# Kernel tuning notes

Hardware: AMD Instinct MI355X
Metric: run time of the kernel (lower is better)

The kernel has to match this reference:

```python
import jax, jax.numpy as jnp
import numpy as np

POS_THR = 0.5      # ROI_POSITIVE_THR
NEG_THR = 0.1      # ROI_NEGATIVE_THR
N_SAMPLES = 256    # ROI_SAMPLES
FG_RATIO = 0.25    # ROI_SAMPLE_RATIO
L1W = 1.0          # RPN.L1WEIGHT_INTERSECTION
NUM_FG = int(N_SAMPLES * FG_RATIO)


def _make_boxes(kxy, kwh, shape):
    # valid [x1,y1,x2,y2] boxes in an ~800px image
    xy = jax.random.uniform(kxy, shape[:-1] + (2,)) * 800.0
    wh = jax.random.uniform(kwh, shape[:-1] + (2,)) * 200.0 + 1.0
    return jnp.concatenate([xy, xy + wh], axis=-1)


def setup_inputs() -> dict:
    key = jax.random.key(0)
    k1, k2, k3, k4 = jax.random.split(key, 4)
    proposals = _make_boxes(k1, k2, (16, 16384, 4))  # [B, N, 4]
    gt_boxes = _make_boxes(k3, k4, (16, 128, 4))     # [B, G, 4]
    return {"proposals": proposals, "gt_boxes": gt_boxes}


def _centrehw(b):
    # [x1,y1,x2,y2] -> [cx,cy,w,h]
    x1, y1, x2, y2 = b[..., 0], b[..., 1], b[..., 2], b[..., 3]
    return jnp.stack([(x1 + x2) * 0.5, (y1 + y2) * 0.5, x2 - x1, y2 - y1], axis=-1)


def _targets(gt_c, roi_c):
    dx = (gt_c[..., 0] - roi_c[..., 0]) / roi_c[..., 2]
    dy = (gt_c[..., 1] - roi_c[..., 1]) / roi_c[..., 3]
    dw = jnp.log(gt_c[..., 2] / roi_c[..., 2])
    dh = jnp.log(gt_c[..., 3] / roi_c[..., 3])
    return jnp.stack([dx, dy, dw, dh], axis=-1)


def _iou(prop, gt):
    # prop [B,N,4], gt [B,G,4] -> IoU [B,N,G]
    p = prop[:, :, None, :]
    g = gt[:, None, :, :]
    ix1 = jnp.maximum(p[..., 0], g[..., 0])
    iy1 = jnp.maximum(p[..., 1], g[..., 1])
    ix2 = jnp.minimum(p[..., 2], g[..., 2])
    iy2 = jnp.minimum(p[..., 3], g[..., 3])
    inter = jnp.clip(ix2 - ix1, 0.0) * jnp.clip(iy2 - iy1, 0.0)
    ap = (p[..., 2] - p[..., 0]) * (p[..., 3] - p[..., 1])
    ag = (g[..., 2] - g[..., 0]) * (g[..., 3] - g[..., 1])
    return inter / jnp.maximum(ap + ag - inter, 1e-8)


def _forward(proposals, gt_boxes):
    B, N, _ = proposals.shape
    iou = _iou(proposals, gt_boxes)                       # [B,N,G]
    max_iou = iou.max(axis=-1)                            # [B,N]
    argmax_gt = iou.argmax(axis=-1).astype(jnp.int32)     # [B,N]
    # classify: 1=fg, 0=bg, -1=ignore
    labels = jnp.where(max_iou >= POS_THR, 1,
                       jnp.where(max_iou < NEG_THR, 0, -1)).astype(jnp.int32)
    # randsample: keep <= NUM_FG positives (random), fill rest with negatives.
    r = jax.random.uniform(jax.random.key(1), (B, N))
    pos = labels == 1
    r_pos = jnp.where(pos, r, -1.0)
    order = jnp.argsort(-r_pos, axis=1)
    ranks = jnp.argsort(order, axis=1)                    # rank among positives by r
    pos_sel = pos & (ranks < NUM_FG)
    prio = jnp.where(pos_sel, 3.0 + r,
                     jnp.where(labels == 0, 2.0 + r,
                               jnp.where(pos, 1.0 + r, r)))
    _, idx = jax.lax.top_k(prio, N_SAMPLES)               # [B,S] sampled proposal ids
    batch_labels = jnp.maximum(jnp.take_along_axis(labels, idx, axis=1), 0)  # [B,S]
    roi_batch = jnp.take_along_axis(proposals, idx[..., None], axis=1)       # [B,S,4]
    sel_gt = jnp.take_along_axis(argmax_gt, idx, axis=1)                     # [B,S]
    gt_batch = jnp.take_along_axis(gt_boxes, sel_gt[..., None], axis=1)      # [B,S,4]
    bbox_targets = _targets(_centrehw(gt_batch), _centrehw(roi_batch))       # [B,S,4]
    in_w = jnp.where((batch_labels == 1)[..., None], L1W, 0.0)
    in_w = jnp.broadcast_to(in_w, bbox_targets.shape)
    out_w = (in_w > 0).astype(jnp.float32)
    return roi_batch, batch_labels, bbox_targets, in_w, out_w


def reference(proposals, gt_boxes):
    return _forward(proposals, gt_boxes)
```

## Files before the change

kernel.cpp:

```cpp
#include <hip/hip_runtime.h>
#include <stdint.h>

#define BATCH 16
#define NPROP 16384
#define NGT   128
#define NSAMP 256
#define NFG   64
#define GCAP  512
#define PCAP  8192
#define HCAP  4096
#define NBLK  64
#define BPB   256
#define LOGB  8

typedef unsigned long long ull;

__device__ __forceinline__ void thr_block(uint32_t c0, uint32_t c1,
                                          uint32_t* o0, uint32_t* o1) {
    const uint32_t k0 = 0u, k1 = 1u, ks2 = 0x1BD11BDBu;
    uint32_t x0 = c0 + k0, x1 = c1 + k1;
#define RND(d) { x0 += x1; x1 = (x1 << d) | (x1 >> (32 - d)); x1 ^= x0; }
    RND(13) RND(15) RND(26) RND(6)   x0 += k1;  x1 += ks2 + 1u;
    RND(17) RND(29) RND(16) RND(24)  x0 += ks2; x1 += k0 + 2u;
    RND(13) RND(15) RND(26) RND(6)   x0 += k0;  x1 += k1 + 3u;
    RND(17) RND(29) RND(16) RND(24)  x0 += k1;  x1 += ks2 + 4u;
    RND(13) RND(15) RND(26) RND(6)   x0 += ks2; x1 += k0 + 5u;
#undef RND
    *o0 = x0; *o1 = x1;
}

__device__ __forceinline__ uint32_t thr_part_xor(uint32_t f) {
    uint32_t a, b; thr_block(0u, f, &a, &b);
    return a ^ b;
}

__global__ void __launch_bounds__(256) k_compute(
    const float* __restrict__ props, const float* __restrict__ gts,
    ull* __restrict__ lists, uint32_t* __restrict__ cntblk)
{
#pragma clang fp contract(off)
    const int b = blockIdx.y;
    const int blk = blockIdx.x;
    const int tid = threadIdx.x;
    const int n = blk * BPB + tid;
    __shared__ float4 g4[NGT];
    __shared__ uint32_t wc[3][4], we_s[3][4];
    if (tid < NGT)
        g4[tid] = ((const float4*)gts)[(size_t)b * NGT + tid];
    __syncthreads();
    const float4 pb = ((const float4*)props)[(size_t)b * NPROP + n];
    const float ap = (pb.z - pb.x) * (pb.w - pb.y);
    float best = -1.0f; int bg = 0;
    #pragma unroll 4
    for (int i = 0; i < NGT; ++i) {
        const float4 gb = g4[i];
        float ag = (gb.z - gb.x) * (gb.w - gb.y);
        float w  = fmaxf(fminf(pb.z, gb.z) - fmaxf(pb.x, gb.x), 0.0f);
        float hh = fmaxf(fminf(pb.w, gb.w) - fmaxf(pb.y, gb.y), 0.0f);
        float inter = w * hh;
        float un = fmaxf(ap + ag - inter, 1e-8f);
        float iou = inter / un;
        if (iou > best) { best = iou; bg = i; }
    }
    uint32_t lab = (best >= 0.5f) ? 2u : ((best < 0.1f) ? 1u : 0u);
    const uint32_t f = (uint32_t)b * NPROP + (uint32_t)n;
    uint32_t mant = thr_part_xor(f) >> 9;
    ull entry = ((ull)(lab == 2u) << 44) | ((ull)mant << 21)
              | ((ull)(16383u - (uint32_t)n) << 7) | (ull)(uint32_t)bg;

    bool cP = (lab == 2u);
    bool cN = (lab == 1u);
    bool cI = (lab == 0u);
    ull mP = __ballot(cP), mN = __ballot(cN), mI = __ballot(cI);
    const int w = tid >> 6;
    const uint32_t lane = (uint32_t)tid & 63u;
    if (lane == 0) {
        wc[0][w] = (uint32_t)__popcll(mP);
        wc[1][w] = (uint32_t)__popcll(mN);
        wc[2][w] = (uint32_t)__popcll(mI);
    }
    __syncthreads();
    if (tid < 3) {
        uint32_t e = 0;
        #pragma unroll
        for (int i = 0; i < 4; i++) { we_s[tid][i] = e; e += wc[tid][i]; }
        cntblk[((size_t)b * NBLK + blk) * 4 + tid] = e;
    }
    __syncthreads();
    ull lt = lane ? (~0ull >> (64u - lane)) : 0ull;
    ull* slab = lists + (size_t)b * 4 * NPROP;
    const uint32_t segB = (uint32_t)blk * BPB;
    if (cP) slab[0 * NPROP + segB + we_s[0][w] + (uint32_t)__popcll(mP & lt)] = entry;
    if (cN) slab[1 * NPROP + segB + we_s[1][w] + (uint32_t)__popcll(mN & lt)] = entry;
    if (cI) slab[2 * NPROP + segB + we_s[2][w] + (uint32_t)__popcll(mI & lt)] = entry;
}

__global__ void __launch_bounds__(1024) k_select(
    const float* __restrict__ props, const float* __restrict__ gts,
    const ull* __restrict__ lists, const uint32_t* __restrict__ cntblk,
    float* __restrict__ out)
{
#pragma clang fp contract(off)
    const int b = blockIdx.x;
    const int tid = threadIdx.x;
    const int wid = tid >> 6;
    const uint32_t lane = (uint32_t)tid & 63u;
    __shared__ ull      dpos[PCAP];
    __shared__ ull      dneg[HCAP];
    __shared__ uint32_t histA[2048];
    __shared__ uint32_t histB[2048];
    __shared__ ull      gatA[GCAP];
    __shared__ ull      gatB[GCAP];
    __shared__ ull      selk[NSAMP];
    __shared__ uint32_t sela[NSAMP];
    __shared__ uint32_t bc[NBLK * 4];
    __shared__ uint32_t preP[NBLK], preN[NBLK], tot[3];
    __shared__ uint32_t shA[3], shB[3], shS[3];
    __shared__ uint32_t gcA, gcB, gcnt, selc;
    __shared__ ull sh_thrA, sh_thrB, sh_thr;

    const ull* Spos = lists + ((size_t)b * 4 + 0) * NPROP;
    const ull* Sneg = lists + ((size_t)b * 4 + 1) * NPROP;
    const ull* Sign = lists + ((size_t)b * 4 + 2) * NPROP;

    if (tid < NBLK * 4) bc[tid] = cntblk[(size_t)b * NBLK * 4 + tid];
    histA[tid] = 0; histA[tid + 1024] = 0;
    histB[tid] = 0; histB[tid + 1024] = 0;
    if (tid == 0) { gcA = 0; gcB = 0; gcnt = 0; selc = 0; }
    __syncthreads();
    if (wid < 3) {
        uint32_t own = bc[lane * 4 + (uint32_t)wid];
        uint32_t v = own;
        #pragma unroll
        for (int off = 1; off < 64; off <<= 1) {
            uint32_t t = (uint32_t)__shfl_up((int)v, off);
            if (lane >= (uint32_t)off) v += t;
        }
        if (wid == 0) preP[lane] = v - own;
        else if (wid == 1) preN[lane] = v - own;
        if (lane == 63) tot[wid] = v;
    }
    __syncthreads();
    const uint32_t npos = tot[0], nneg = tot[1], nig = tot[2];
    const uint32_t npn  = npos + nneg;
    const uint32_t c3   = (npos < NFG) ? npos : NFG;
    const uint32_t k2   = NSAMP - c3;
    const bool dP = (npos <= PCAP), dH = (nneg <= HCAP);
    const bool fast0 = (npn >= NSAMP) && (c3 + nneg >= NSAMP) && dP && dH;

    auto keyA_of = [](ull e) -> ull {
        return (((e >> 21) & 0x7FFFFFull) << 14) | ((e >> 7) & 0x3FFFull);
    };
    auto keyB_neg = [](ull ent) -> ull {
        uint32_t mant = (uint32_t)((ent >> 21) & 0x7FFFFFull);
        uint32_t invn = (uint32_t)((ent >> 7) & 0x3FFFull);
        float r = __uint_as_float(0x3F800000u | mant) - 1.0f;
        float prio = 2.0f + r;
        return (((ull)__float_as_uint(prio)) << 14) | (ull)invn;
    };
    auto keyB_ign = [](ull ent) -> ull {
        uint32_t mant = (uint32_t)((ent >> 21) & 0x7FFFFFull);
        uint32_t invn = (uint32_t)((ent >> 7) & 0x3FFFull);
        float r = __uint_as_float(0x3F800000u | mant) - 1.0f;
        float prio = 0.0f + r;
        return (((ull)__float_as_uint(prio)) << 14) | (ull)invn;
    };
    ull thrA = 0;
    auto keyB_pos = [&](ull ent) -> ull {
        uint32_t mant = (uint32_t)((ent >> 21) & 0x7FFFFFull);
        uint32_t invn = (uint32_t)((ent >> 7) & 0x3FFFull);
        float r = __uint_as_float(0x3F800000u | mant) - 1.0f;
        uint32_t cls = (keyA_of(ent) >= thrA) ? 3u : 1u;
        float prio = (float)cls + r;
        return (((ull)__float_as_uint(prio)) << 14) | (ull)invn;
    };
    auto push = [&](ull key, ull ent, uint32_t fg) {
        uint32_t s = atomicAdd(&selc, 1u);
        if (s < NSAMP) { selk[s] = key; sela[s] = (fg << 7) | (uint32_t)(ent & 0x7Full); }
    };

    for (int s4 = 0; s4 < 4; ++s4) {
        uint32_t seg = (uint32_t)(wid * 4 + s4);
        if (dP) {
            uint32_t c = bc[seg * 4 + 0], bb = preP[seg];
            for (uint32_t i = lane; i < c; i += 64) {
                ull ent = Spos[seg * BPB + i];
                dpos[bb + i] = ent;
                if (fast0 && npos > NFG)
                    atomicAdd(&histA[(uint32_t)(keyA_of(ent) >> 26) & 2047u], 1u);
            }
        }
        if (dH) {
            uint32_t c = bc[seg * 4 + 1], bb = preN[seg];
            for (uint32_t i = lane; i < c; i += 64) {
                ull ent = Sneg[seg * BPB + i];
                dneg[bb + i] = ent;
                if (fast0)
                    atomicAdd(&histB[(uint32_t)(keyB_neg(ent) >> 26) & 2047u], 1u);
            }
        }
    }
    __syncthreads();

    auto locW = [&](const uint32_t* h, uint32_t k, uint32_t* o3) {
        uint32_t cs = 0;
        if (lane < 32) {
            const uint32_t base = lane * 64u;
            #pragma unroll 8
            for (uint32_t i = 0; i < 64; i++) cs += h[base + ((i + lane) & 63u)];
        }
        uint32_t s = cs;
        #pragma unroll
        for (int off = 1; off < 32; off <<= 1) {
            uint32_t t = __shfl_down(s, off);
            if (lane + off < 32) s += t;
        }
        uint32_t sExcl = s - cs;
        bool cond = (lane < 32) && (sExcl < k) && (k <= s);
        ull ball = __ballot(cond);
        uint32_t cstar = (uint32_t)(__ffsll((unsigned long long)ball) - 1);
        uint32_t kc_ = (uint32_t)__shfl((int)(k - sExcl), (int)cstar);
        uint32_t val = h[cstar * 64u + lane];
        uint32_t fi = val;
        #pragma unroll
        for (int off = 1; off < 64; off <<= 1) {
            uint32_t t = __shfl_down(fi, off);
            if (lane + off < 64) fi += t;
        }
        uint32_t fExcl = fi - val;
        bool cond2 = (fExcl < kc_) && (kc_ <= fi);
        ull ball2 = __ballot(cond2);
        uint32_t bstar = (uint32_t)(__ffsll((unsigned long long)ball2) - 1);
        if (lane == bstar) { o3[0] = cstar * 64u + lane; o3[1] = kc_ - fExcl; o3[2] = val; }
    };

    bool fast = fast0;
    if (fast) {
        if (wid == 0 && npos > NFG) locW(histA, NFG, shA);
        if (wid == 1)               locW(histB, k2,  shB);
        __syncthreads();
        if ((npos > NFG && shA[2] > GCAP) || (shB[2] > GCAP)) fast = false;
    }
    if (fast) {
        if (npos > NFG) {
            uint32_t digA = shA[0];
            for (uint32_t j = tid; j < npos; j += 1024) {
                ull k = keyA_of(dpos[j]);
                if (((uint32_t)(k >> 26) & 2047u) == digA) gatA[atomicAdd(&gcA, 1u)] = k;
            }
        }
        {
            uint32_t digB = shB[0];
            for (uint32_t j = tid; j < nneg; j += 1024) {
                ull k = keyB_neg(dneg[j]);
                if (((uint32_t)(k >> 26) & 2047u) == digB) gatB[atomicAdd(&gcB, 1u)] = k;
            }
        }
        __syncthreads();
        if (npos > NFG) {
            if ((uint32_t)tid < gcA) {
                ull x = gatA[tid]; uint32_t r = 0;
                for (uint32_t j = 0; j < gcA; j++) r += (gatA[j] > x);
                if (r == shA[1] - 1) sh_thrA = x;
            }
        } else if (tid == 0) sh_thrA = 0;
        if (tid >= 512 && (uint32_t)(tid - 512) < gcB) {
            ull x = gatB[tid - 512]; uint32_t r = 0;
            for (uint32_t j = 0; j < gcB; j++) r += (gatB[j] > x);
            if (r == shB[1] - 1) sh_thrB = x;
        }
        __syncthreads();
        thrA = sh_thrA;
        const ull thrB = sh_thrB;
        for (uint32_t j = tid; j < npos; j += 1024) {
            ull ent = dpos[j];
            if (keyA_of(ent) >= thrA) push(keyB_pos(ent), ent, 1u);
        }
        for (uint32_t j = tid; j < nneg; j += 1024) {
            ull ent = dneg[j];
            ull k = keyB_neg(ent);
            if (k >= thrB) push(k, ent, 0u);
        }
        __syncthreads();
    }
    if (!fast) {
        const uint32_t MSEG = NBLK * BPB;
        const uint32_t mPos = dP ? npos : MSEG;
        const uint32_t mNeg = dH ? nneg : MSEG;
        auto posEnt = [&](uint32_t j, bool& e) -> ull {
            if (dP) { e = true; return dpos[j]; }
            e = (j & (BPB - 1u)) < bc[(j >> LOGB) * 4 + 0];
            return e ? Spos[j] : 0ull;
        };
        auto negEnt = [&](uint32_t j, bool& e) -> ull {
            if (dH) { e = true; return dneg[j]; }
            e = (j & (BPB - 1u)) < bc[(j >> LOGB) * 4 + 1];
            return e ? Sneg[j] : 0ull;
        };
        auto igEnt = [&](uint32_t j, bool& e) -> ull {
            e = (j & (BPB - 1u)) < bc[(j >> LOGB) * 4 + 2];
            return e ? Sign[j] : 0ull;
        };
        auto radix = [&](auto&& kf, uint32_t m, uint32_t k, int shift) -> ull {
            if (m <= GCAP) {
                if (tid == 0) gcnt = 0;
                __syncthreads();
                for (uint32_t j = tid; j < m; j += 1024) {
                    bool e; ull key = kf(j, e);
                    if (e) { uint32_t s = atomicAdd(&gcnt, 1u); gatA[s] = key; }
                }
                __syncthreads();
                uint32_t gc = gcnt;
                if ((uint32_t)tid < gc) {
                    ull x = gatA[tid]; uint32_t r = 0;
                    for (uint32_t j = 0; j < gc; j++) r += (gatA[j] > x);
                    if (r == k - 1) sh_thr = x;
                }
                __syncthreads();
                return sh_thr;
            }
            ull prefix = 0, mask = 0;
            for (;;) {
                histA[tid] = 0; histA[tid + 1024] = 0;
                __syncthreads();
                for (uint32_t j = tid; j < m; j += 1024) {
                    bool e; ull key = kf(j, e);
                    if (e && ((key ^ prefix) & mask) == 0)
                        atomicAdd(&histA[(uint32_t)(key >> shift) & 2047u], 1u);
                }
                __syncthreads();
                if (tid < 64) locW(histA, k, shS);
                __syncthreads();
                uint32_t dig = shS[0], kk = shS[1], cnt = shS[2];
                prefix |= ((ull)dig) << shift;
                mask   |= 2047ull << shift;
                if (cnt <= GCAP || shift == 0) {
                    if (tid == 0) gcnt = 0;
                    __syncthreads();
                    for (uint32_t j = tid; j < m; j += 1024) {
                        bool e; ull key = kf(j, e);
                        if (e && ((key ^ prefix) & mask) == 0) {
                            uint32_t s = atomicAdd(&gcnt, 1u);
                            if (s < GCAP) gatA[s] = key;
                        }
                    }
                    __syncthreads();
                    uint32_t gc = (gcnt < GCAP) ? gcnt : GCAP;
                    if ((uint32_t)tid < gc) {
                        ull x = gatA[tid]; uint32_t r = 0;
                        for (uint32_t j = 0; j < gc; j++) r += (gatA[j] > x);
                        if (r == kk - 1) sh_thr = x;
                    }
                    __syncthreads();
                    return sh_thr;
                } else {
                    k = kk;
                    shift = (shift >= 11) ? shift - 11 : 0;
                    __syncthreads();
                }
            }
        };

        if (npos > NFG) {
            thrA = radix([&](uint32_t j, bool& e) -> ull {
                ull ent = posEnt(j, e); return keyA_of(ent); }, mPos, NFG, 26);
        }
        uint32_t clsStar = (npn >= NSAMP) ? ((NSAMP <= c3 + nneg) ? 2u : 1u) : 0u;
        ull thrB = 0;
        if (clsStar == 2u) {
            thrB = radix([&](uint32_t j, bool& e) -> ull {
                ull ent = negEnt(j, e); return keyB_neg(ent); }, mNeg, k2, 26);
        } else if (clsStar == 1u) {
            thrB = radix([&](uint32_t j, bool& e) -> ull {
                ull ent = posEnt(j, e);
                ull kb = keyB_pos(ent);
                e = e && ((kb >> 14) < 0x40000000ull);
                return kb; }, mPos, NSAMP - c3 - nneg, 26);
        } else {
            thrB = radix([&](uint32_t j, bool& e) -> ull {
                ull ent = igEnt(j, e); return keyB_ign(ent); }, MSEG, NSAMP - npn, 34);
        }
        __syncthreads();
        for (uint32_t j = tid; j < mPos; j += 1024) {
            bool e; ull ent = posEnt(j, e);
            if (!e) continue;
            ull key = keyB_pos(ent);
            if (clsStar == 0u || key >= thrB) push(key, ent, 1u);
        }
        for (uint32_t j = tid; j < mNeg; j += 1024) {
            bool e; ull ent = negEnt(j, e);
            if (!e) continue;
            ull key = keyB_neg(ent);
            if (clsStar == 0u || key >= thrB) push(key, ent, 0u);
        }
        if (clsStar == 0u) {
            for (uint32_t j = tid; j < MSEG; j += 1024) {
                bool e; ull ent = igEnt(j, e);
                if (!e) continue;
                ull key = keyB_ign(ent);
                if (key >= thrB) push(key, ent, 0u);
            }
        }
        __syncthreads();
    }

    if (tid < NSAMP) {
        ull x = selk[tid];
        uint32_t r = 0;
        for (int j = 0; j < NSAMP; j++) r += (selk[j] > x);
        uint32_t n = 16383u - (uint32_t)(x & 0x3FFFull);
        uint32_t aux = sela[tid];
        uint32_t bg = aux & 0x7Fu;
        const int isfg = (int)((aux >> 7) & 1u);
        const float4 pb = ((const float4*)props)[(size_t)b * NPROP + n];
        const float4 gb = ((const float4*)gts)[(size_t)b * NGT + bg];
        const size_t O_ROI = 0;
        const size_t O_LBL = (size_t)BATCH * NSAMP * 4;
        const size_t O_TGT = O_LBL + (size_t)BATCH * NSAMP;
        const size_t O_INW = O_TGT + (size_t)BATCH * NSAMP * 4;
        const size_t O_OUW = O_INW + (size_t)BATCH * NSAMP * 4;
        const size_t row = (size_t)b * NSAMP + r;
        out[O_ROI + row * 4 + 0] = pb.x;
        out[O_ROI + row * 4 + 1] = pb.y;
        out[O_ROI + row * 4 + 2] = pb.z;
        out[O_ROI + row * 4 + 3] = pb.w;
        out[O_LBL + row] = isfg ? 1.0f : 0.0f;
        float rw  = pb.z - pb.x, rh = pb.w - pb.y;
        float gw  = gb.z - gb.x, gh = gb.w - gb.y;
        out[O_TGT + row * 4 + 0] = ((gb.x + gb.z) * 0.5f - (pb.x + pb.z) * 0.5f) / rw;
        out[O_TGT + row * 4 + 1] = ((gb.y + gb.w) * 0.5f - (pb.y + pb.w) * 0.5f) / rh;
        out[O_TGT + row * 4 + 2] = logf(gw / rw);
        out[O_TGT + row * 4 + 3] = logf(gh / rh);
        float wv = isfg ? 1.0f : 0.0f;
        for (int c = 0; c < 4; c++) {
            out[O_INW + row * 4 + c] = wv;
            out[O_OUW + row * 4 + c] = wv;
        }
    }
}

extern "C" void kernel_launch(void* const* d_in, const int* in_sizes, int n_in,
                              void* d_out, int out_size, void* d_ws, size_t ws_size,
                              hipStream_t stream) {
    (void)in_sizes; (void)n_in; (void)out_size; (void)ws_size;
    const float* props = (const float*)d_in[0];
    const float* gts   = (const float*)d_in[1];
    ull* lists = (ull*)d_ws;
    uint32_t* cntblk = (uint32_t*)((char*)d_ws + (size_t)BATCH * 4 * NPROP * 8);
    float* out = (float*)d_out;

    dim3 gridA(NBLK, BATCH);
    k_compute<<<gridA, 256, 0, stream>>>(props, gts, lists, cntblk);
    k_select<<<BATCH, 1024, 0, stream>>>(props, gts, lists, cntblk, out);
}
```

Measured before the change: 99.08 us.

## Split negatives into high/low random-key buckets to shrink select staging

The compute kernel now partitions negative proposals by their random mantissa into a high bucket (mant >= threshold) and a low bucket, writing four lists instead of three. The select kernel stages only the high-key negatives in shared memory, with the staging buffer halved, and runs its histogram radix select over that smaller set when it holds enough candidates. The low bucket is read only in the fallback path. This is meant to cut global reads, atomics and LDS traffic in the select stage, at the cost of an extra ballot and output list, plus a more complex fallback path.

Result: no change. 97.81 us (-1.3%).

```diff
diff --git a/kernel.cpp b/kernel.cpp
--- a/kernel.cpp
+++ b/kernel.cpp
@@ -8,10 +8,11 @@
 #define NFG   64
 #define GCAP  512
 #define PCAP  8192
-#define HCAP  4096
+#define HCAP  2048
 #define NBLK  64
 #define BPB   256
 #define LOGB  8
+#define NEGT  0x780002u
 
 typedef unsigned long long ull;
 
@@ -44,7 +45,7 @@
     const int tid = threadIdx.x;
     const int n = blk * BPB + tid;
     __shared__ float4 g4[NGT];
-    __shared__ uint32_t wc[3][4], we_s[3][4];
+    __shared__ uint32_t wc[4][4], we_s[4][4];
     if (tid < NGT)
         g4[tid] = ((const float4*)gts)[(size_t)b * NGT + tid];
     __syncthreads();
@@ -69,18 +70,20 @@
               | ((ull)(16383u - (uint32_t)n) << 7) | (ull)(uint32_t)bg;
 
     bool cP = (lab == 2u);
-    bool cN = (lab == 1u);
+    bool cH = (lab == 1u) && (mant >= NEGT);
+    bool cL = (lab == 1u) && (mant <  NEGT);
     bool cI = (lab == 0u);
-    ull mP = __ballot(cP), mN = __ballot(cN), mI = __ballot(cI);
+    ull mP = __ballot(cP), mH = __ballot(cH), mL = __ballot(cL), mI = __ballot(cI);
     const int w = tid >> 6;
     const uint32_t lane = (uint32_t)tid & 63u;
     if (lane == 0) {
         wc[0][w] = (uint32_t)__popcll(mP);
-        wc[1][w] = (uint32_t)__popcll(mN);
-        wc[2][w] = (uint32_t)__popcll(mI);
-    }
-    __syncthreads();
-    if (tid < 3) {
+        wc[1][w] = (uint32_t)__popcll(mH);
+        wc[2][w] = (uint32_t)__popcll(mL);
+        wc[3][w] = (uint32_t)__popcll(mI);
+    }
+    __syncthreads();
+    if (tid < 4) {
         uint32_t e = 0;
         #pragma unroll
         for (int i = 0; i < 4; i++) { we_s[tid][i] = e; e += wc[tid][i]; }
@@ -91,8 +94,9 @@
     ull* slab = lists + (size_t)b * 4 * NPROP;
     const uint32_t segB = (uint32_t)blk * BPB;
     if (cP) slab[0 * NPROP + segB + we_s[0][w] + (uint32_t)__popcll(mP & lt)] = entry;
-    if (cN) slab[1 * NPROP + segB + we_s[1][w] + (uint32_t)__popcll(mN & lt)] = entry;
-    if (cI) slab[2 * NPROP + segB + we_s[2][w] + (uint32_t)__popcll(mI & lt)] = entry;
+    if (cH) slab[1 * NPROP + segB + we_s[1][w] + (uint32_t)__popcll(mH & lt)] = entry;
+    if (cL) slab[2 * NPROP + segB + we_s[2][w] + (uint32_t)__popcll(mL & lt)] = entry;
+    if (cI) slab[3 * NPROP + segB + we_s[3][w] + (uint32_t)__popcll(mI & lt)] = entry;
 }
 
 __global__ void __launch_bounds__(1024) k_select(
@@ -106,7 +110,7 @@
     const int wid = tid >> 6;
     const uint32_t lane = (uint32_t)tid & 63u;
     __shared__ ull      dpos[PCAP];
-    __shared__ ull      dneg[HCAP];
+    __shared__ ull      dnh[HCAP];
     __shared__ uint32_t histA[2048];
     __shared__ uint32_t histB[2048];
     __shared__ ull      gatA[GCAP];
@@ -114,21 +118,22 @@
     __shared__ ull      selk[NSAMP];
     __shared__ uint32_t sela[NSAMP];
     __shared__ uint32_t bc[NBLK * 4];
-    __shared__ uint32_t preP[NBLK], preN[NBLK], tot[3];
+    __shared__ uint32_t preP[NBLK], preH[NBLK], tot[4];
     __shared__ uint32_t shA[3], shB[3], shS[3];
     __shared__ uint32_t gcA, gcB, gcnt, selc;
     __shared__ ull sh_thrA, sh_thrB, sh_thr;
 
     const ull* Spos = lists + ((size_t)b * 4 + 0) * NPROP;
-    const ull* Sneg = lists + ((size_t)b * 4 + 1) * NPROP;
-    const ull* Sign = lists + ((size_t)b * 4 + 2) * NPROP;
+    const ull* SnH  = lists + ((size_t)b * 4 + 1) * NPROP;
+    const ull* SnL  = lists + ((size_t)b * 4 + 2) * NPROP;
+    const ull* Sign = lists + ((size_t)b * 4 + 3) * NPROP;
 
     if (tid < NBLK * 4) bc[tid] = cntblk[(size_t)b * NBLK * 4 + tid];
     histA[tid] = 0; histA[tid + 1024] = 0;
     histB[tid] = 0; histB[tid + 1024] = 0;
     if (tid == 0) { gcA = 0; gcB = 0; gcnt = 0; selc = 0; }
     __syncthreads();
-    if (wid < 3) {
+    if (wid < 4) {
         uint32_t own = bc[lane * 4 + (uint32_t)wid];
         uint32_t v = own;
         #pragma unroll
@@ -137,16 +142,17 @@
             if (lane >= (uint32_t)off) v += t;
         }
         if (wid == 0) preP[lane] = v - own;
-        else if (wid == 1) preN[lane] = v - own;
+        else if (wid == 1) preH[lane] = v - own;
         if (lane == 63) tot[wid] = v;
     }
     __syncthreads();
-    const uint32_t npos = tot[0], nneg = tot[1], nig = tot[2];
+    const uint32_t npos = tot[0], nH = tot[1], nL = tot[2], nig = tot[3];
+    const uint32_t nneg = nH + nL;
     const uint32_t npn  = npos + nneg;
     const uint32_t c3   = (npos < NFG) ? npos : NFG;
     const uint32_t k2   = NSAMP - c3;
-    const bool dP = (npos <= PCAP), dH = (nneg <= HCAP);
-    const bool fast0 = (npn >= NSAMP) && (c3 + nneg >= NSAMP) && dP && dH;
+    const bool dP = (npos <= PCAP), dH = (nH <= HCAP);
+    const bool fast0 = (npn >= NSAMP) && (c3 + nneg >= NSAMP) && dP && dH && (nH >= k2);
 
     auto keyA_of = [](ull e) -> ull {
         return (((e >> 21) & 0x7FFFFFull) << 14) | ((e >> 7) & 0x3FFFull);
@@ -191,10 +197,10 @@
             }
         }
         if (dH) {
-            uint32_t c = bc[seg * 4 + 1], bb = preN[seg];
+            uint32_t c = bc[seg * 4 + 1], bb = preH[seg];
             for (uint32_t i = lane; i < c; i += 64) {
-                ull ent = Sneg[seg * BPB + i];
-                dneg[bb + i] = ent;
+                ull ent = SnH[seg * BPB + i];
+                dnh[bb + i] = ent;
                 if (fast0)
                     atomicAdd(&histB[(uint32_t)(keyB_neg(ent) >> 26) & 2047u], 1u);
             }
@@ -251,8 +257,8 @@
         }
         {
             uint32_t digB = shB[0];
-            for (uint32_t j = tid; j < nneg; j += 1024) {
-                ull k = keyB_neg(dneg[j]);
+            for (uint32_t j = tid; j < nH; j += 1024) {
+                ull k = keyB_neg(dnh[j]);
                 if (((uint32_t)(k >> 26) & 2047u) == digB) gatB[atomicAdd(&gcB, 1u)] = k;
             }
         }
@@ -276,8 +282,8 @@
             ull ent = dpos[j];
             if (keyA_of(ent) >= thrA) push(keyB_pos(ent), ent, 1u);
         }
-        for (uint32_t j = tid; j < nneg; j += 1024) {
-            ull ent = dneg[j];
+        for (uint32_t j = tid; j < nH; j += 1024) {
+            ull ent = dnh[j];
             ull k = keyB_neg(ent);
             if (k >= thrB) push(k, ent, 0u);
         }
@@ -286,19 +292,23 @@
     if (!fast) {
         const uint32_t MSEG = NBLK * BPB;
         const uint32_t mPos = dP ? npos : MSEG;
-        const uint32_t mNeg = dH ? nneg : MSEG;
+        const uint32_t mH   = dH ? nH   : MSEG;
         auto posEnt = [&](uint32_t j, bool& e) -> ull {
             if (dP) { e = true; return dpos[j]; }
             e = (j & (BPB - 1u)) < bc[(j >> LOGB) * 4 + 0];
             return e ? Spos[j] : 0ull;
         };
-        auto negEnt = [&](uint32_t j, bool& e) -> ull {
-            if (dH) { e = true; return dneg[j]; }
+        auto nhEnt = [&](uint32_t j, bool& e) -> ull {
+            if (dH) { e = true; return dnh[j]; }
             e = (j & (BPB - 1u)) < bc[(j >> LOGB) * 4 + 1];
-            return e ? Sneg[j] : 0ull;
+            return e ? SnH[j] : 0ull;
+        };
+        auto nlEnt = [&](uint32_t j, bool& e) -> ull {
+            e = (j & (BPB - 1u)) < bc[(j >> LOGB) * 4 + 2];
+            return e ? SnL[j] : 0ull;
         };
         auto igEnt = [&](uint32_t j, bool& e) -> ull {
-            e = (j & (BPB - 1u)) < bc[(j >> LOGB) * 4 + 2];
+            e = (j & (BPB - 1u)) < bc[(j >> LOGB) * 4 + 3];
             return e ? Sign[j] : 0ull;
         };
         auto radix = [&](auto&& kf, uint32_t m, uint32_t k, int shift) -> ull {
@@ -366,10 +376,19 @@
                 ull ent = posEnt(j, e); return keyA_of(ent); }, mPos, NFG, 26);
         }
         uint32_t clsStar = (npn >= NSAMP) ? ((NSAMP <= c3 + nneg) ? 2u : 1u) : 0u;
+        bool scanL = true;
         ull thrB = 0;
         if (clsStar == 2u) {
-            thrB = radix([&](uint32_t j, bool& e) -> ull {
-                ull ent = negEnt(j, e); return keyB_neg(ent); }, mNeg, k2, 26);
+            if (nH >= k2) {
+                scanL = false;
+                thrB = radix([&](uint32_t j, bool& e) -> ull {
+                    ull ent = nhEnt(j, e); return keyB_neg(ent); }, mH, k2, 26);
+            } else {
+                thrB = radix([&](uint32_t j, bool& e) -> ull {
+                    if (j < mH) { ull ent = nhEnt(j, e); return keyB_neg(ent); }
+                    ull ent = nlEnt(j - mH, e); return keyB_neg(ent); },
+                    mH + MSEG, k2, 26);
+            }
         } else if (clsStar == 1u) {
             thrB = radix([&](uint32_t j, bool& e) -> ull {
                 ull ent = posEnt(j, e);
@@ -387,11 +406,19 @@
             ull key = keyB_pos(ent);
             if (clsStar == 0u || key >= thrB) push(key, ent, 1u);
         }
-        for (uint32_t j = tid; j < mNeg; j += 1024) {
-            bool e; ull ent = negEnt(j, e);
+        for (uint32_t j = tid; j < mH; j += 1024) {
+            bool e; ull ent = nhEnt(j, e);
             if (!e) continue;
             ull key = keyB_neg(ent);
             if (clsStar == 0u || key >= thrB) push(key, ent, 0u);
+        }
+        if (scanL) {
+            for (uint32_t j = tid; j < MSEG; j += 1024) {
+                bool e; ull ent = nlEnt(j, e);
+                if (!e) continue;
+                ull key = keyB_neg(ent);
+                if (clsStar == 0u || key >= thrB) push(key, ent, 0u);
+            }
         }
         if (clsStar == 0u) {
             for (uint32_t j = tid; j < MSEG; j += 1024) {
```
